# Kernel tuning notes

Hardware: AMD Instinct MI355X
Metric: run time of the kernel (lower is better)

## Reference

```python
import jax, jax.numpy as jnp
import numpy as np

N = 12500      # nodes
E = 200000     # edges (avg degree 16)
IN = 32        # inp_dim
OUT = 32       # out_dim
ATTN = 32      # attn_rel_emb_dim
R = 200        # num_rels
NB = 50        # num_bases


def setup_inputs() -> dict:
    key = jax.random.key(0)
    ks = jax.random.split(key, 10)
    node_feat = jax.random.normal(ks[0], (N, IN), jnp.float32)
    total_edge = jax.random.randint(ks[1], (2, E), 0, N)
    total_target_relation = jax.random.normal(ks[2], (E, ATTN), jnp.float32)
    total_relation_embed = jax.random.normal(ks[3], (E, ATTN), jnp.float32)
    total_relation = jax.random.randint(ks[4], (E,), 0, R)
    # learned parameters (xavier-ish scale)
    weight = jax.random.normal(ks[5], (NB, IN, OUT), jnp.float32) * 0.1
    w_comp = jax.random.normal(ks[6], (R, NB), jnp.float32) * 0.1
    self_loop_weight = jax.random.normal(ks[7], (IN, OUT), jnp.float32) * 0.1
    A_w = jax.random.normal(ks[8], (IN, 2 * IN + 2 * ATTN), jnp.float32) * 0.1
    A_b = jnp.zeros((IN,), jnp.float32)
    B_w = jax.random.normal(ks[9], (1, IN), jnp.float32) * 0.1
    B_b = jnp.zeros((1,), jnp.float32)
    return {
        'node_feat': node_feat,
        'total_target_relation': total_target_relation,
        'total_relation_embed': total_relation_embed,
        'weight': weight,
        'w_comp': w_comp,
        'self_loop_weight': self_loop_weight,
        'A_w': A_w,
        'A_b': A_b,
        'B_w': B_w,
        'B_b': B_b,
        'total_edge': total_edge,
        'total_relation': total_relation,
    }


def reference(node_feat, total_target_relation, total_relation_embed,
              weight, w_comp, self_loop_weight, A_w, A_b, B_w, B_b,
              total_edge, total_relation):
    # basis decomposition: per-relation weight [R, IN, OUT]
    rel_w = jnp.einsum('rb,bio->rio', w_comp, weight)
    src = node_feat[total_edge[0]]            # [E, IN]
    tgt = node_feat[total_edge[1]]            # [E, IN]
    # per-edge relation-specific transform (bmm in torch)
    msg = jnp.einsum('ei,eio->eo', src, rel_w[total_relation])  # [E, OUT]
    curr = tgt @ self_loop_weight             # [E, OUT]
    # attention MLP: sigmoid(B(relu(A(concat))))
    e = jnp.concatenate([src, tgt, total_relation_embed, total_target_relation], axis=1)
    h = jax.nn.relu(e @ A_w.T + A_b)
    a = jax.nn.sigmoid(h @ B_w.T + B_b)       # [E, 1]
    curr = curr + msg * a
    # gnn_spmm(e2n_sp, curr): scatter-add edge messages to target nodes
    out = jax.ops.segment_sum(curr, total_edge[1], num_segments=node_feat.shape[0])
    return out  # [N, OUT]
```

## Files before the change

kernel.cpp:

```cpp
#include <hip/hip_runtime.h>

#define N_NODES 12500
#define N_EDGES 200000
#define DIM 32
#define N_REL 200
#define N_BASES 50

#define OUT_ELEMS   (N_NODES * DIM)
#define ZERO_BLOCKS ((OUT_ELEMS + 1023) / 1024)

#define PE_MAX 203008
#define N_DUMMY_BLOCKS 8

#define NB_BLK 196
#define CHUNK 1024

#define HIST_BASE (N_REL + 1 + ZERO_BLOCKS)
#define PREP_BLOCKS (HIST_BASE + NB_BLK)
#define EDGE_BLOCKS (PE_MAX / 256)

#define AWBF_OFF  (N_REL * 1024 * 2)
#define SLWT_OFF  (AWBF_OFF + 32 * 128 * 2)
#define BCT_OFF   (SLWT_OFF + 32 * 32 * 2)
#define BBT_OFF   (BCT_OFF + N_REL * NB_BLK * 4)
#define OFFS_OFF  (BBT_OFF + N_REL * NB_BLK * 4)
#define TOTS_OFF  (OFFS_OFF + 816)
#define SLOT_OFF  (TOTS_OFF + 800)

typedef __attribute__((ext_vector_type(8))) short short8;
typedef __attribute__((ext_vector_type(4))) float f32x4;

__device__ __forceinline__ unsigned short f2bf(float x) {
    union { float f; unsigned u; } v; v.f = x;
    unsigned r = (v.u + 0x7FFFu + ((v.u >> 16) & 1u)) >> 16;
    return (unsigned short)r;
}

__device__ __forceinline__ short8 cvt8(float4 a, float4 b) {
    short8 r;
    r[0] = (short)f2bf(a.x); r[1] = (short)f2bf(a.y);
    r[2] = (short)f2bf(a.z); r[3] = (short)f2bf(a.w);
    r[4] = (short)f2bf(b.x); r[5] = (short)f2bf(b.y);
    r[6] = (short)f2bf(b.z); r[7] = (short)f2bf(b.w);
    return r;
}

#define MFMA(A, B, C) __builtin_amdgcn_mfma_f32_16x16x32_bf16(A, B, C, 0, 0, 0)

__global__ __launch_bounds__(256) void prep_kernel(
    const float* __restrict__ weight,
    const float* __restrict__ w_comp,
    const float* __restrict__ Aw,
    const float* __restrict__ slw,
    const int*  __restrict__ rel,
    unsigned short* __restrict__ relwT_bf,
    unsigned short* __restrict__ aw_bf,
    unsigned short* __restrict__ slwT_bf,
    int* __restrict__ blockCountsT,
    float* __restrict__ out)
{
    int b = blockIdx.x, tid = threadIdx.x;
    if (b < N_REL) {
        __shared__ float wc[N_BASES];
        if (tid < N_BASES) wc[tid] = w_comp[b * N_BASES + tid];
        __syncthreads();
        const float* wp = weight + tid * 4;
        float4 acc = make_float4(0.f, 0.f, 0.f, 0.f);
        #pragma unroll 10
        for (int bb = 0; bb < N_BASES; bb++) {
            float4 w = *(const float4*)(wp + bb * 1024);
            float c = wc[bb];
            acc.x = fmaf(c, w.x, acc.x); acc.y = fmaf(c, w.y, acc.y);
            acc.z = fmaf(c, w.z, acc.z); acc.w = fmaf(c, w.w, acc.w);
        }
        int i  = tid >> 3;
        int o0 = (tid * 4) & 31;
        unsigned short* dst = relwT_bf + b * 1024 + i;
        dst[(o0 + 0) * 32] = f2bf(acc.x);
        dst[(o0 + 1) * 32] = f2bf(acc.y);
        dst[(o0 + 2) * 32] = f2bf(acc.z);
        dst[(o0 + 3) * 32] = f2bf(acc.w);
    } else if (b == N_REL) {
        for (int x = tid; x < 32 * 128; x += 256) aw_bf[x] = f2bf(Aw[x]);
        for (int x = tid; x < 32 * 32; x += 256) {
            int i = x >> 5, j = x & 31;
            slwT_bf[j * 32 + i] = f2bf(slw[x]);
        }
    } else if (b < HIST_BASE) {
        int base = (b - (N_REL + 1)) * 1024 + tid * 4;
        if (base + 3 < OUT_ELEMS)
            *(float4*)(out + base) = make_float4(0.f, 0.f, 0.f, 0.f);
        else
            for (int k = 0; k < 4; k++)
                if (base + k < OUT_ELEMS) out[base + k] = 0.f;
    } else {
        __shared__ int h[N_REL];
        int blk = b - HIST_BASE;
        for (int x = tid; x < N_REL; x += 256) h[x] = 0;
        __syncthreads();
        int e0 = blk * CHUNK;
        int e1 = e0 + CHUNK; if (e1 > N_EDGES) e1 = N_EDGES;
        for (int e = e0 + tid; e < e1; e += 256) {
            int r = rel[e]; r = r < 0 ? 0 : (r >= N_REL ? N_REL - 1 : r);
            atomicAdd(&h[r], 1);
        }
        __syncthreads();
        for (int x = tid; x < N_REL; x += 256)
            blockCountsT[x * NB_BLK + blk] = h[x];
    }
}

__global__ __launch_bounds__(256) void scan_kernel(
    const int* __restrict__ blockCountsT,
    int* __restrict__ blockBaseT,
    int* __restrict__ offs, int* __restrict__ tots)
{
    __shared__ int s0[256];
    __shared__ int pval[256];
    int tid = threadIdx.x;
    int tot = 0;
    if (tid < N_REL) {
        const int4* cp = (const int4*)(blockCountsT + tid * NB_BLK);
        #pragma unroll 7
        for (int b = 0; b < NB_BLK / 4; b++) {
            int4 c = cp[b];
            tot += c.x + c.y + c.z + c.w;
        }
    }
    int p = (tid < N_REL) ? ((tot + 15) & ~15) : 0;
    pval[tid] = p;
    s0[tid] = p;
    __syncthreads();
    #pragma unroll
    for (int d = 1; d < 256; d <<= 1) {
        int v = s0[tid];
        if (tid >= d) v += s0[tid - d];
        __syncthreads();
        s0[tid] = v;
        __syncthreads();
    }
    int off = s0[tid] - pval[tid];
    if (tid < N_REL) { offs[tid] = off; tots[tid] = tot; }
    if (tid == 255) offs[N_REL] = s0[255];
    if (tid < N_REL) {
        const int4* cp = (const int4*)(blockCountsT + tid * NB_BLK);
        int4* bp = (int4*)(blockBaseT + tid * NB_BLK);
        int run = off;
        #pragma unroll 7
        for (int b = 0; b < NB_BLK / 4; b++) {
            int4 c = cp[b];
            int4 w;
            w.x = run;
            w.y = w.x + c.x;
            w.z = w.y + c.y;
            w.w = w.z + c.z;
            run = w.w + c.w;
            bp[b] = w;
        }
    }
}

__global__ __launch_bounds__(256) void gatescatter_kernel(
    const float* __restrict__ node_feat,
    const float* __restrict__ ttr,
    const float* __restrict__ tre,
    const float* __restrict__ Ab,
    const float* __restrict__ Bw,
    const float* __restrict__ Bb,
    const int*  __restrict__ edge0,
    const int*  __restrict__ edge1,
    const int*  __restrict__ rel,
    const unsigned short* __restrict__ aw_bf,
    const int* __restrict__ blockBaseT,
    const int* __restrict__ offs, const int* __restrict__ tots,
    int4* __restrict__ slot4)
{
    int b = blockIdx.x, tid = threadIdx.x;
    if (b >= NB_BLK) {
        int db = b - NB_BLK;
        const int4 dummy = make_int4(0, -1, 0, 0);
        for (int r = db; r < N_REL; r += N_DUMMY_BLOCKS) {
            int start = offs[r] + tots[r];
            int end   = offs[r] + ((tots[r] + 15) & ~15);
            for (int j = start + tid; j < end; j += 256)
                slot4[j] = dummy;
        }
        int padTotal = offs[N_REL];
        for (int j = padTotal + db * 256 + tid; j < PE_MAX; j += N_DUMMY_BLOCKS * 256)
            slot4[j] = dummy;
        return;
    }

    __shared__ int cur[N_REL];
    for (int x = tid; x < N_REL; x += 256)
        cur[x] = blockBaseT[x * NB_BLK + b];
    __syncthreads();

    int wave = tid >> 6;
    int lane = tid & 63;
    int m = lane & 15;
    int q = lane >> 4;

    short8 bA[4][2];
    #pragma unroll
    for (int hh = 0; hh < 2; hh++)
        #pragma unroll
        for (int c = 0; c < 4; c++)
            bA[c][hh] = *(const short8*)(aw_bf + (16 * hh + m) * 128 + 32 * c + 8 * q);
    float ab0 = Ab[m], ab1 = Ab[16 + m];
    float bw0 = Bw[m], bw1 = Bw[16 + m], Bb0 = Bb[0];

    int c0 = b * CHUNK;
    int cend = c0 + CHUNK; if (cend > N_EDGES) cend = N_EDGES;
    for (int it = 0; it < CHUNK / 256; it++) {
        int ebase = c0 + it * 256 + wave * 64;
        if (ebase >= cend) continue;

        int e_lane = ebase + lane;
        int s_ld = edge0[e_lane]; s_ld = s_ld < 0 ? 0 : (s_ld >= N_NODES ? N_NODES - 1 : s_ld);
        int t_ld = edge1[e_lane]; t_ld = t_ld < 0 ? 0 : (t_ld >= N_NODES ? N_NODES - 1 : t_ld);
        int r_ld = rel[e_lane];   r_ld = r_ld < 0 ? 0 : (r_ld >= N_REL   ? N_REL   - 1 : r_ld);

        short8 fsrc[4], ftgt[4], fre_[4], ftr_[4];
        #pragma unroll
        for (int g = 0; g < 4; g++) {
            int s_m = __shfl(s_ld, g * 16 + m, 64);
            int t_m = __shfl(t_ld, g * 16 + m, 64);
            int e_m = ebase + g * 16 + m;
            const float* sp = node_feat + s_m * DIM + q * 8;
            float4 sv0 = *(const float4*)sp, sv1 = *(const float4*)(sp + 4);
            const float* tp = node_feat + t_m * DIM + q * 8;
            float4 tv0 = *(const float4*)tp, tv1 = *(const float4*)(tp + 4);
            const float* rp = tre + e_m * DIM + q * 8;
            float4 rv0 = *(const float4*)rp, rv1 = *(const float4*)(rp + 4);
            const float* qp = ttr + e_m * DIM + q * 8;
            float4 qv0 = *(const float4*)qp, qv1 = *(const float4*)(qp + 4);
            fsrc[g] = cvt8(sv0, sv1);
            ftgt[g] = cvt8(tv0, tv1);
            fre_[g] = cvt8(rv0, rv1);
            ftr_[g] = cvt8(qv0, qv1);
        }

        #pragma unroll
        for (int g = 0; g < 4; g++) {
            f32x4 h0 = {ab0, ab0, ab0, ab0};
            f32x4 h1 = {ab1, ab1, ab1, ab1};
            h0 = MFMA(fsrc[g], bA[0][0], h0);  h1 = MFMA(fsrc[g], bA[0][1], h1);
            h0 = MFMA(ftgt[g], bA[1][0], h0);  h1 = MFMA(ftgt[g], bA[1][1], h1);
            h0 = MFMA(fre_[g], bA[2][0], h0);  h1 = MFMA(fre_[g], bA[2][1], h1);
            h0 = MFMA(ftr_[g], bA[3][0], h0);  h1 = MFMA(ftr_[g], bA[3][1], h1);

            float av[4];
            #pragma unroll
            for (int v = 0; v < 4; v++) {
                float p = fmaxf(h0[v], 0.f) * bw0 + fmaxf(h1[v], 0.f) * bw1;
                p += __shfl_xor(p, 1, 16);
                p += __shfl_xor(p, 2, 16);
                p += __shfl_xor(p, 4, 16);
                p += __shfl_xor(p, 8, 16);
                av[v] = 1.f / (1.f + __expf(-(p + Bb0)));
            }
            int j = g * 16 + 4 * q + m;
            int s_j = __shfl(s_ld, j, 64);
            int t_j = __shfl(t_ld, j, 64);
            int r_j = __shfl(r_ld, j, 64);
            float a_j = (m == 0) ? av[0] : (m == 1) ? av[1]
                      : (m == 2) ? av[2] : av[3];
            if (m < 4) {
                int pos = atomicAdd(&cur[r_j], 1);
                slot4[pos] = make_int4(s_j, t_j, __float_as_int(a_j), r_j);
            }
        }
    }
}

__global__ __launch_bounds__(256) void edge_kernel(
    const float* __restrict__ node_feat,
    const int4* __restrict__ slot4,
    const unsigned short* __restrict__ relwT_bf,
    const unsigned short* __restrict__ slwT_bf,
    float* __restrict__ out)
{
    int tid  = threadIdx.x;
    int wave = tid >> 6;
    int lane = tid & 63;
    int m = lane & 15;
    int q = lane >> 4;
    int wbase = blockIdx.x * 256 + wave * 64;

    int4 v = slot4[wbase + lane];
    int s_ld = v.x, t_ld = v.y, a_ld = v.z, r_ld = v.w;

    short8 bS[2];
    bS[0] = *(const short8*)(slwT_bf + m * 32 + 8 * q);
    bS[1] = *(const short8*)(slwT_bf + (16 + m) * 32 + 8 * q);

    short8 fsrc[4], ftgt[4], bM[4][2];
    #pragma unroll
    for (int g = 0; g < 4; g++) {
        int r_g = __shfl(r_ld, g * 16, 64);
        int s_m = __shfl(s_ld, g * 16 + m, 64);
        int t_m = __shfl(t_ld, g * 16 + m, 64);
        int t_mc = t_m < 0 ? 0 : t_m;
        const float* sp = node_feat + s_m * DIM + q * 8;
        float4 sv0 = *(const float4*)sp, sv1 = *(const float4*)(sp + 4);
        const float* tp = node_feat + t_mc * DIM + q * 8;
        float4 tv0 = *(const float4*)tp, tv1 = *(const float4*)(tp + 4);
        fsrc[g] = cvt8(sv0, sv1);
        ftgt[g] = cvt8(tv0, tv1);
        bM[g][0] = *(const short8*)(relwT_bf + r_g * 1024 + m * 32 + 8 * q);
        bM[g][1] = *(const short8*)(relwT_bf + r_g * 1024 + (16 + m) * 32 + 8 * q);
    }

    #pragma unroll
    for (int g = 0; g < 4; g++) {
        f32x4 m0 = {0.f, 0.f, 0.f, 0.f};
        f32x4 m1 = {0.f, 0.f, 0.f, 0.f};
        f32x4 c0 = {0.f, 0.f, 0.f, 0.f};
        f32x4 c1 = {0.f, 0.f, 0.f, 0.f};
        m0 = MFMA(fsrc[g], bM[g][0], m0);
        m1 = MFMA(fsrc[g], bM[g][1], m1);
        c0 = MFMA(ftgt[g], bS[0], c0);
        c1 = MFMA(ftgt[g], bS[1], c1);
        #pragma unroll
        for (int vv = 0; vv < 4; vv++) {
            int row = 4 * q + vv;
            int tv = __shfl(t_ld, g * 16 + row, 64);
            float a_row = __int_as_float(__shfl(a_ld, g * 16 + row, 64));
            if (tv >= 0) {
                atomicAdd(&out[tv * DIM + m],      c0[vv] + m0[vv] * a_row);
                atomicAdd(&out[tv * DIM + 16 + m], c1[vv] + m1[vv] * a_row);
            }
        }
    }
}

extern "C" void kernel_launch(void* const* d_in, const int* in_sizes, int n_in,
                              void* d_out, int out_size, void* d_ws, size_t ws_size,
                              hipStream_t stream) {
    const float* node_feat = (const float*)d_in[0];
    const float* ttr       = (const float*)d_in[1];
    const float* tre       = (const float*)d_in[2];
    const float* weight    = (const float*)d_in[3];
    const float* w_comp    = (const float*)d_in[4];
    const float* slw       = (const float*)d_in[5];
    const float* Aw        = (const float*)d_in[6];
    const float* Ab        = (const float*)d_in[7];
    const float* Bw        = (const float*)d_in[8];
    const float* Bb        = (const float*)d_in[9];
    const int*  total_edge = (const int*)d_in[10];
    const int*  rel        = (const int*)d_in[11];
    const int*  edge0 = total_edge;
    const int*  edge1 = total_edge + N_EDGES;

    char* ws = (char*)d_ws;
    unsigned short* relwT_bf = (unsigned short*)ws;
    unsigned short* aw_bf    = (unsigned short*)(ws + AWBF_OFF);
    unsigned short* slwT_bf  = (unsigned short*)(ws + SLWT_OFF);
    int*  blockCountsT = (int*)(ws + BCT_OFF);
    int*  blockBaseT   = (int*)(ws + BBT_OFF);
    int*  offs         = (int*)(ws + OFFS_OFF);
    int*  tots         = (int*)(ws + TOTS_OFF);
    int4* slot4        = (int4*)(ws + SLOT_OFF);
    float* out = (float*)d_out;

    prep_kernel<<<PREP_BLOCKS, 256, 0, stream>>>(
        weight, w_comp, Aw, slw, rel, relwT_bf, aw_bf, slwT_bf,
        blockCountsT, out);

    scan_kernel<<<1, 256, 0, stream>>>(blockCountsT, blockBaseT, offs, tots);

    gatescatter_kernel<<<NB_BLK + N_DUMMY_BLOCKS, 256, 0, stream>>>(
        node_feat, ttr, tre, Ab, Bw, Bb, edge0, edge1, rel,
        aw_bf, blockBaseT, offs, tots, slot4);

    edge_kernel<<<EDGE_BLOCKS, 256, 0, stream>>>(
        node_feat, slot4, relwT_bf, slwT_bf, out);
}
```

Measured before the change: 172.3 us.

## Fuse scan, gate/scatter and edge kernels into one persistent kernel

Merges the scan, the gate/scatter pass and the edge MFMA pass into a single persistent kernel of 256 blocks. Block 0 does the scan and publishes a flag. The other blocks compute attention gates into shared memory while the scan runs, then scatter edges into relation-sorted slots, pass a global atomic barrier, and finish the edge transform with a grid-stride loop. It also re-chunks the edges into 241 chunks of 832 to balance work. The aim is to remove two kernel launches and overlap the scan with the gate computation, at the cost of spin-wait barriers that need all blocks to be co-resident.

```diff
diff --git a/kernel.cpp b/kernel.cpp
--- a/kernel.cpp
+++ b/kernel.cpp
@@ -7,25 +7,31 @@
 #define N_BASES 50
 
 #define OUT_ELEMS   (N_NODES * DIM)
-#define ZERO_BLOCKS ((OUT_ELEMS + 1023) / 1024)
+#define ZERO_BLOCKS 391
 
 #define PE_MAX 203008
-#define N_DUMMY_BLOCKS 8
-
-#define NB_BLK 196
-#define CHUNK 1024
+
+#define CPG 13
+#define CHUNK (CPG * 64)
+#define NGROUPS 3125
+#define NB_CHUNK 241
+#define NB_PAD 244
+
+#define MEGA_BLK 256
+#define EDGE_UNITS (PE_MAX / 64)
+#define N_DUMMY_WRITERS (MEGA_BLK - NB_CHUNK)
 
 #define HIST_BASE (N_REL + 1 + ZERO_BLOCKS)
-#define PREP_BLOCKS (HIST_BASE + NB_BLK)
-#define EDGE_BLOCKS (PE_MAX / 256)
+#define PREP_BLOCKS (HIST_BASE + NB_CHUNK)
 
 #define AWBF_OFF  (N_REL * 1024 * 2)
 #define SLWT_OFF  (AWBF_OFF + 32 * 128 * 2)
 #define BCT_OFF   (SLWT_OFF + 32 * 32 * 2)
-#define BBT_OFF   (BCT_OFF + N_REL * NB_BLK * 4)
-#define OFFS_OFF  (BBT_OFF + N_REL * NB_BLK * 4)
+#define BBT_OFF   (BCT_OFF + N_REL * NB_PAD * 4)
+#define OFFS_OFF  (BBT_OFF + N_REL * NB_PAD * 4)
 #define TOTS_OFF  (OFFS_OFF + 816)
-#define SLOT_OFF  (TOTS_OFF + 800)
+#define FLAG_OFF  (TOTS_OFF + 800)
+#define SLOT_OFF  (FLAG_OFF + 16)
 
 typedef __attribute__((ext_vector_type(8))) short short8;
 typedef __attribute__((ext_vector_type(4))) float f32x4;
@@ -57,6 +63,7 @@
     unsigned short* __restrict__ aw_bf,
     unsigned short* __restrict__ slwT_bf,
     int* __restrict__ blockCountsT,
+    int* __restrict__ flags,
     float* __restrict__ out)
 {
     int b = blockIdx.x, tid = threadIdx.x;
@@ -86,6 +93,11 @@
             int i = x >> 5, j = x & 31;
             slwT_bf[j * 32 + i] = f2bf(slw[x]);
         }
+        if (tid < 4) flags[tid] = 0;
+        for (int x = tid; x < N_REL * (NB_PAD - NB_CHUNK); x += 256) {
+            int r = x / (NB_PAD - NB_CHUNK), p = x % (NB_PAD - NB_CHUNK);
+            blockCountsT[r * NB_PAD + NB_CHUNK + p] = 0;
+        }
     } else if (b < HIST_BASE) {
         int base = (b - (N_REL + 1)) * 1024 + tid * 4;
         if (base + 3 < OUT_ELEMS)
@@ -95,10 +107,10 @@
                 if (base + k < OUT_ELEMS) out[base + k] = 0.f;
     } else {
         __shared__ int h[N_REL];
-        int blk = b - HIST_BASE;
+        int c = b - HIST_BASE;
         for (int x = tid; x < N_REL; x += 256) h[x] = 0;
         __syncthreads();
-        int e0 = blk * CHUNK;
+        int e0 = c * CHUNK;
         int e1 = e0 + CHUNK; if (e1 > N_EDGES) e1 = N_EDGES;
         for (int e = e0 + tid; e < e1; e += 256) {
             int r = rel[e]; r = r < 0 ? 0 : (r >= N_REL ? N_REL - 1 : r);
@@ -106,61 +118,11 @@
         }
         __syncthreads();
         for (int x = tid; x < N_REL; x += 256)
-            blockCountsT[x * NB_BLK + blk] = h[x];
+            blockCountsT[x * NB_PAD + c] = h[x];
     }
 }
 
-__global__ __launch_bounds__(256) void scan_kernel(
-    const int* __restrict__ blockCountsT,
-    int* __restrict__ blockBaseT,
-    int* __restrict__ offs, int* __restrict__ tots)
-{
-    __shared__ int s0[256];
-    __shared__ int pval[256];
-    int tid = threadIdx.x;
-    int tot = 0;
-    if (tid < N_REL) {
-        const int4* cp = (const int4*)(blockCountsT + tid * NB_BLK);
-        #pragma unroll 7
-        for (int b = 0; b < NB_BLK / 4; b++) {
-            int4 c = cp[b];
-            tot += c.x + c.y + c.z + c.w;
-        }
-    }
-    int p = (tid < N_REL) ? ((tot + 15) & ~15) : 0;
-    pval[tid] = p;
-    s0[tid] = p;
-    __syncthreads();
-    #pragma unroll
-    for (int d = 1; d < 256; d <<= 1) {
-        int v = s0[tid];
-        if (tid >= d) v += s0[tid - d];
-        __syncthreads();
-        s0[tid] = v;
-        __syncthreads();
-    }
-    int off = s0[tid] - pval[tid];
-    if (tid < N_REL) { offs[tid] = off; tots[tid] = tot; }
-    if (tid == 255) offs[N_REL] = s0[255];
-    if (tid < N_REL) {
-        const int4* cp = (const int4*)(blockCountsT + tid * NB_BLK);
-        int4* bp = (int4*)(blockBaseT + tid * NB_BLK);
-        int run = off;
-        #pragma unroll 7
-        for (int b = 0; b < NB_BLK / 4; b++) {
-            int4 c = cp[b];
-            int4 w;
-            w.x = run;
-            w.y = w.x + c.x;
-            w.z = w.y + c.y;
-            w.w = w.z + c.z;
-            run = w.w + c.w;
-            bp[b] = w;
-        }
-    }
-}
-
-__global__ __launch_bounds__(256) void gatescatter_kernel(
+__global__ __launch_bounds__(256, 2) void mega_kernel(
     const float* __restrict__ node_feat,
     const float* __restrict__ ttr,
     const float* __restrict__ tre,
@@ -171,165 +133,231 @@
     const int*  __restrict__ edge1,
     const int*  __restrict__ rel,
     const unsigned short* __restrict__ aw_bf,
-    const int* __restrict__ blockBaseT,
-    const int* __restrict__ offs, const int* __restrict__ tots,
-    int4* __restrict__ slot4)
+    const unsigned short* __restrict__ relwT_bf,
+    const unsigned short* __restrict__ slwT_bf,
+    const int* __restrict__ blockCountsT,
+    int* __restrict__ blockBaseT,
+    int* __restrict__ offs, int* __restrict__ tots,
+    int* __restrict__ flags,
+    int4* __restrict__ slot4,
+    float* __restrict__ out)
 {
     int b = blockIdx.x, tid = threadIdx.x;
-    if (b >= NB_BLK) {
-        int db = b - NB_BLK;
+    int wave = tid >> 6;
+    int lane = tid & 63;
+    int m = lane & 15;
+    int q = lane >> 4;
+
+    __shared__ float a_stash[CHUNK];
+    __shared__ int   cur[N_REL];
+    __shared__ int   s0[256];
+    __shared__ int   pval[256];
+
+    int* scanflag = flags;
+    int* bar      = flags + 1;
+
+    if (b == 0) {
+        int tot = 0;
+        if (tid < N_REL) {
+            const int4* cp = (const int4*)(blockCountsT + tid * NB_PAD);
+            for (int c = 0; c < NB_PAD / 4; c++) {
+                int4 v = cp[c];
+                tot += v.x + v.y + v.z + v.w;
+            }
+        }
+        int p = (tid < N_REL) ? ((tot + 15) & ~15) : 0;
+        pval[tid] = p;
+        s0[tid] = p;
+        __syncthreads();
+        #pragma unroll
+        for (int d = 1; d < 256; d <<= 1) {
+            int v = s0[tid];
+            if (tid >= d) v += s0[tid - d];
+            __syncthreads();
+            s0[tid] = v;
+            __syncthreads();
+        }
+        int off = s0[tid] - pval[tid];
+        if (tid < N_REL) { offs[tid] = off; tots[tid] = tot; }
+        if (tid == 255) offs[N_REL] = s0[255];
+        if (tid < N_REL) {
+            const int4* cp = (const int4*)(blockCountsT + tid * NB_PAD);
+            int4* bp = (int4*)(blockBaseT + tid * NB_PAD);
+            int run = off;
+            for (int c = 0; c < NB_PAD / 4; c++) {
+                int4 v = cp[c];
+                int4 w;
+                w.x = run;
+                w.y = w.x + v.x;
+                w.z = w.y + v.y;
+                w.w = w.z + v.z;
+                run = w.w + v.w;
+                bp[c] = w;
+            }
+        }
+        __syncthreads();
+        if (tid == 0) {
+            __threadfence();
+            __hip_atomic_store(scanflag, 1, __ATOMIC_RELEASE, __HIP_MEMORY_SCOPE_AGENT);
+        }
+    }
+
+    int g_lo = b * CPG;
+    int g_cnt = 0;
+    if (b < NB_CHUNK) {
+        g_cnt = NGROUPS - g_lo; if (g_cnt > CPG) g_cnt = CPG;
+
+        short8 bA[4][2];
+        #pragma unroll
+        for (int hh = 0; hh < 2; hh++)
+            #pragma unroll
+            for (int c = 0; c < 4; c++)
+                bA[c][hh] = *(const short8*)(aw_bf + (16 * hh + m) * 128 + 32 * c + 8 * q);
+        float ab0 = Ab[m], ab1 = Ab[16 + m];
+        float bw0 = Bw[m], bw1 = Bw[16 + m], Bb0 = Bb[0];
+
+        for (int gi = wave; gi < g_cnt; gi += 4) {
+            int ebase = (g_lo + gi) * 64;
+            int e_lane = ebase + lane;
+            int s_ld = edge0[e_lane]; s_ld = s_ld < 0 ? 0 : (s_ld >= N_NODES ? N_NODES - 1 : s_ld);
+            int t_ld = edge1[e_lane]; t_ld = t_ld < 0 ? 0 : (t_ld >= N_NODES ? N_NODES - 1 : t_ld);
+
+            short8 fsrc[4], ftgt[4], fre_[4], ftr_[4];
+            #pragma unroll
+            for (int g = 0; g < 4; g++) {
+                int s_m = __shfl(s_ld, g * 16 + m, 64);
+                int t_m = __shfl(t_ld, g * 16 + m, 64);
+                int e_m = ebase + g * 16 + m;
+                const float* sp = node_feat + s_m * DIM + q * 8;
+                float4 sv0 = *(const float4*)sp, sv1 = *(const float4*)(sp + 4);
+                const float* tp = node_feat + t_m * DIM + q * 8;
+                float4 tv0 = *(const float4*)tp, tv1 = *(const float4*)(tp + 4);
+                const float* rp = tre + e_m * DIM + q * 8;
+                float4 rv0 = *(const float4*)rp, rv1 = *(const float4*)(rp + 4);
+                const float* qp = ttr + e_m * DIM + q * 8;
+                float4 qv0 = *(const float4*)qp, qv1 = *(const float4*)(qp + 4);
+                fsrc[g] = cvt8(sv0, sv1);
+                ftgt[g] = cvt8(tv0, tv1);
+                fre_[g] = cvt8(rv0, rv1);
+                ftr_[g] = cvt8(qv0, qv1);
+            }
+
+            #pragma unroll
+            for (int g = 0; g < 4; g++) {
+                f32x4 h0 = {ab0, ab0, ab0, ab0};
+                f32x4 h1 = {ab1, ab1, ab1, ab1};
+                h0 = MFMA(fsrc[g], bA[0][0], h0);  h1 = MFMA(fsrc[g], bA[0][1], h1);
+                h0 = MFMA(ftgt[g], bA[1][0], h0);  h1 = MFMA(ftgt[g], bA[1][1], h1);
+                h0 = MFMA(fre_[g], bA[2][0], h0);  h1 = MFMA(fre_[g], bA[2][1], h1);
+                h0 = MFMA(ftr_[g], bA[3][0], h0);  h1 = MFMA(ftr_[g], bA[3][1], h1);
+
+                float av[4];
+                #pragma unroll
+                for (int v = 0; v < 4; v++) {
+                    float p = fmaxf(h0[v], 0.f) * bw0 + fmaxf(h1[v], 0.f) * bw1;
+                    p += __shfl_xor(p, 1, 16);
+                    p += __shfl_xor(p, 2, 16);
+                    p += __shfl_xor(p, 4, 16);
+                    p += __shfl_xor(p, 8, 16);
+                    av[v] = 1.f / (1.f + __expf(-(p + Bb0)));
+                }
+                float a_j = (m == 0) ? av[0] : (m == 1) ? av[1]
+                          : (m == 2) ? av[2] : av[3];
+                if (m < 4) a_stash[gi * 64 + g * 16 + 4 * q + m] = a_j;
+            }
+        }
+    }
+
+    __syncthreads();
+    if (tid == 0)
+        while (__hip_atomic_load(scanflag, __ATOMIC_ACQUIRE, __HIP_MEMORY_SCOPE_AGENT) == 0)
+            __builtin_amdgcn_s_sleep(2);
+    __syncthreads();
+    __threadfence();
+
+    if (b < NB_CHUNK) {
+        for (int x = tid; x < N_REL; x += 256)
+            cur[x] = blockBaseT[x * NB_PAD + b];
+        __syncthreads();
+        int c0 = g_lo * 64;
+        int clen = g_cnt * 64;
+        for (int ei = tid; ei < clen; ei += 256) {
+            int e = c0 + ei;
+            int r = rel[e];   r = r < 0 ? 0 : (r >= N_REL   ? N_REL   - 1 : r);
+            int s = edge0[e]; s = s < 0 ? 0 : (s >= N_NODES ? N_NODES - 1 : s);
+            int t = edge1[e]; t = t < 0 ? 0 : (t >= N_NODES ? N_NODES - 1 : t);
+            int pos = atomicAdd(&cur[r], 1);
+            slot4[pos] = make_int4(s, t, __float_as_int(a_stash[ei]), r);
+        }
+    } else {
+        int db = b - NB_CHUNK;
         const int4 dummy = make_int4(0, -1, 0, 0);
-        for (int r = db; r < N_REL; r += N_DUMMY_BLOCKS) {
+        for (int r = db; r < N_REL; r += N_DUMMY_WRITERS) {
             int start = offs[r] + tots[r];
             int end   = offs[r] + ((tots[r] + 15) & ~15);
             for (int j = start + tid; j < end; j += 256)
                 slot4[j] = dummy;
         }
         int padTotal = offs[N_REL];
-        for (int j = padTotal + db * 256 + tid; j < PE_MAX; j += N_DUMMY_BLOCKS * 256)
+        for (int j = padTotal + db * 256 + tid; j < PE_MAX; j += N_DUMMY_WRITERS * 256)
             slot4[j] = dummy;
-        return;
-    }
-
-    __shared__ int cur[N_REL];
-    for (int x = tid; x < N_REL; x += 256)
-        cur[x] = blockBaseT[x * NB_BLK + b];
+    }
+
     __syncthreads();
-
-    int wave = tid >> 6;
-    int lane = tid & 63;
-    int m = lane & 15;
-    int q = lane >> 4;
-
-    short8 bA[4][2];
-    #pragma unroll
-    for (int hh = 0; hh < 2; hh++)
-        #pragma unroll
-        for (int c = 0; c < 4; c++)
-            bA[c][hh] = *(const short8*)(aw_bf + (16 * hh + m) * 128 + 32 * c + 8 * q);
-    float ab0 = Ab[m], ab1 = Ab[16 + m];
-    float bw0 = Bw[m], bw1 = Bw[16 + m], Bb0 = Bb[0];
-
-    int c0 = b * CHUNK;
-    int cend = c0 + CHUNK; if (cend > N_EDGES) cend = N_EDGES;
-    for (int it = 0; it < CHUNK / 256; it++) {
-        int ebase = c0 + it * 256 + wave * 64;
-        if (ebase >= cend) continue;
-
-        int e_lane = ebase + lane;
-        int s_ld = edge0[e_lane]; s_ld = s_ld < 0 ? 0 : (s_ld >= N_NODES ? N_NODES - 1 : s_ld);
-        int t_ld = edge1[e_lane]; t_ld = t_ld < 0 ? 0 : (t_ld >= N_NODES ? N_NODES - 1 : t_ld);
-        int r_ld = rel[e_lane];   r_ld = r_ld < 0 ? 0 : (r_ld >= N_REL   ? N_REL   - 1 : r_ld);
-
-        short8 fsrc[4], ftgt[4], fre_[4], ftr_[4];
-        #pragma unroll
-        for (int g = 0; g < 4; g++) {
-            int s_m = __shfl(s_ld, g * 16 + m, 64);
-            int t_m = __shfl(t_ld, g * 16 + m, 64);
-            int e_m = ebase + g * 16 + m;
-            const float* sp = node_feat + s_m * DIM + q * 8;
-            float4 sv0 = *(const float4*)sp, sv1 = *(const float4*)(sp + 4);
-            const float* tp = node_feat + t_m * DIM + q * 8;
-            float4 tv0 = *(const float4*)tp, tv1 = *(const float4*)(tp + 4);
-            const float* rp = tre + e_m * DIM + q * 8;
-            float4 rv0 = *(const float4*)rp, rv1 = *(const float4*)(rp + 4);
-            const float* qp = ttr + e_m * DIM + q * 8;
-            float4 qv0 = *(const float4*)qp, qv1 = *(const float4*)(qp + 4);
-            fsrc[g] = cvt8(sv0, sv1);
-            ftgt[g] = cvt8(tv0, tv1);
-            fre_[g] = cvt8(rv0, rv1);
-            ftr_[g] = cvt8(qv0, qv1);
-        }
-
-        #pragma unroll
-        for (int g = 0; g < 4; g++) {
-            f32x4 h0 = {ab0, ab0, ab0, ab0};
-            f32x4 h1 = {ab1, ab1, ab1, ab1};
-            h0 = MFMA(fsrc[g], bA[0][0], h0);  h1 = MFMA(fsrc[g], bA[0][1], h1);
-            h0 = MFMA(ftgt[g], bA[1][0], h0);  h1 = MFMA(ftgt[g], bA[1][1], h1);
-            h0 = MFMA(fre_[g], bA[2][0], h0);  h1 = MFMA(fre_[g], bA[2][1], h1);
-            h0 = MFMA(ftr_[g], bA[3][0], h0);  h1 = MFMA(ftr_[g], bA[3][1], h1);
-
-            float av[4];
-            #pragma unroll
-            for (int v = 0; v < 4; v++) {
-                float p = fmaxf(h0[v], 0.f) * bw0 + fmaxf(h1[v], 0.f) * bw1;
-                p += __shfl_xor(p, 1, 16);
-                p += __shfl_xor(p, 2, 16);
-                p += __shfl_xor(p, 4, 16);
-                p += __shfl_xor(p, 8, 16);
-                av[v] = 1.f / (1.f + __expf(-(p + Bb0)));
-            }
-            int j = g * 16 + 4 * q + m;
-            int s_j = __shfl(s_ld, j, 64);
-            int t_j = __shfl(t_ld, j, 64);
-            int r_j = __shfl(r_ld, j, 64);
-            float a_j = (m == 0) ? av[0] : (m == 1) ? av[1]
-                      : (m == 2) ? av[2] : av[3];
-            if (m < 4) {
-                int pos = atomicAdd(&cur[r_j], 1);
-                slot4[pos] = make_int4(s_j, t_j, __float_as_int(a_j), r_j);
-            }
-        }
-    }
-}
-
-__global__ __launch_bounds__(256) void edge_kernel(
-    const float* __restrict__ node_feat,
-    const int4* __restrict__ slot4,
-    const unsigned short* __restrict__ relwT_bf,
-    const unsigned short* __restrict__ slwT_bf,
-    float* __restrict__ out)
-{
-    int tid  = threadIdx.x;
-    int wave = tid >> 6;
-    int lane = tid & 63;
-    int m = lane & 15;
-    int q = lane >> 4;
-    int wbase = blockIdx.x * 256 + wave * 64;
-
-    int4 v = slot4[wbase + lane];
-    int s_ld = v.x, t_ld = v.y, a_ld = v.z, r_ld = v.w;
+    if (tid == 0) {
+        __threadfence();
+        __hip_atomic_fetch_add(bar, 1, __ATOMIC_ACQ_REL, __HIP_MEMORY_SCOPE_AGENT);
+        while (__hip_atomic_load(bar, __ATOMIC_ACQUIRE, __HIP_MEMORY_SCOPE_AGENT) < MEGA_BLK)
+            __builtin_amdgcn_s_sleep(2);
+    }
+    __syncthreads();
+    __threadfence();
 
     short8 bS[2];
     bS[0] = *(const short8*)(slwT_bf + m * 32 + 8 * q);
     bS[1] = *(const short8*)(slwT_bf + (16 + m) * 32 + 8 * q);
 
-    short8 fsrc[4], ftgt[4], bM[4][2];
-    #pragma unroll
-    for (int g = 0; g < 4; g++) {
-        int r_g = __shfl(r_ld, g * 16, 64);
-        int s_m = __shfl(s_ld, g * 16 + m, 64);
-        int t_m = __shfl(t_ld, g * 16 + m, 64);
-        int t_mc = t_m < 0 ? 0 : t_m;
-        const float* sp = node_feat + s_m * DIM + q * 8;
-        float4 sv0 = *(const float4*)sp, sv1 = *(const float4*)(sp + 4);
-        const float* tp = node_feat + t_mc * DIM + q * 8;
-        float4 tv0 = *(const float4*)tp, tv1 = *(const float4*)(tp + 4);
-        fsrc[g] = cvt8(sv0, sv1);
-        ftgt[g] = cvt8(tv0, tv1);
-        bM[g][0] = *(const short8*)(relwT_bf + r_g * 1024 + m * 32 + 8 * q);
-        bM[g][1] = *(const short8*)(relwT_bf + r_g * 1024 + (16 + m) * 32 + 8 * q);
-    }
-
-    #pragma unroll
-    for (int g = 0; g < 4; g++) {
-        f32x4 m0 = {0.f, 0.f, 0.f, 0.f};
-        f32x4 m1 = {0.f, 0.f, 0.f, 0.f};
-        f32x4 c0 = {0.f, 0.f, 0.f, 0.f};
-        f32x4 c1 = {0.f, 0.f, 0.f, 0.f};
-        m0 = MFMA(fsrc[g], bM[g][0], m0);
-        m1 = MFMA(fsrc[g], bM[g][1], m1);
-        c0 = MFMA(ftgt[g], bS[0], c0);
-        c1 = MFMA(ftgt[g], bS[1], c1);
+    for (int u = b * 4 + wave; u < EDGE_UNITS; u += MEGA_BLK * 4) {
+        int wbase = u * 64;
+        int4 v = slot4[wbase + lane];
+        int s_ld = v.x, t_ld = v.y, a_ld = v.z, r_ld = v.w;
+
+        short8 fsrc[4], ftgt[4], bM[4][2];
         #pragma unroll
-        for (int vv = 0; vv < 4; vv++) {
-            int row = 4 * q + vv;
-            int tv = __shfl(t_ld, g * 16 + row, 64);
-            float a_row = __int_as_float(__shfl(a_ld, g * 16 + row, 64));
-            if (tv >= 0) {
-                atomicAdd(&out[tv * DIM + m],      c0[vv] + m0[vv] * a_row);
-                atomicAdd(&out[tv * DIM + 16 + m], c1[vv] + m1[vv] * a_row);
+        for (int g = 0; g < 4; g++) {
+            int r_g = __shfl(r_ld, g * 16, 64);
+            int s_m = __shfl(s_ld, g * 16 + m, 64);
+            int t_m = __shfl(t_ld, g * 16 + m, 64);
+            int t_mc = t_m < 0 ? 0 : t_m;
+            const float* sp = node_feat + s_m * DIM + q * 8;
+            float4 sv0 = *(const float4*)sp, sv1 = *(const float4*)(sp + 4);
+            const float* tp = node_feat + t_mc * DIM + q * 8;
+            float4 tv0 = *(const float4*)tp, tv1 = *(const float4*)(tp + 4);
+            fsrc[g] = cvt8(sv0, sv1);
+            ftgt[g] = cvt8(tv0, tv1);
+            bM[g][0] = *(const short8*)(relwT_bf + r_g * 1024 + m * 32 + 8 * q);
+            bM[g][1] = *(const short8*)(relwT_bf + r_g * 1024 + (16 + m) * 32 + 8 * q);
+        }
+
+        #pragma unroll
+        for (int g = 0; g < 4; g++) {
+            f32x4 m0 = {0.f, 0.f, 0.f, 0.f};
+            f32x4 m1 = {0.f, 0.f, 0.f, 0.f};
+            f32x4 c0 = {0.f, 0.f, 0.f, 0.f};
+            f32x4 c1 = {0.f, 0.f, 0.f, 0.f};
+            m0 = MFMA(fsrc[g], bM[g][0], m0);
+            m1 = MFMA(fsrc[g], bM[g][1], m1);
+            c0 = MFMA(ftgt[g], bS[0], c0);
+            c1 = MFMA(ftgt[g], bS[1], c1);
+            #pragma unroll
+            for (int vv = 0; vv < 4; vv++) {
+                int row = 4 * q + vv;
+                int tv = __shfl(t_ld, g * 16 + row, 64);
+                float a_row = __int_as_float(__shfl(a_ld, g * 16 + row, 64));
+                if (tv >= 0) {
+                    atomicAdd(&out[tv * DIM + m],      c0[vv] + m0[vv] * a_row);
+                    atomicAdd(&out[tv * DIM + 16 + m], c1[vv] + m1[vv] * a_row);
+                }
             }
         }
     }
@@ -361,19 +389,16 @@
     int*  blockBaseT   = (int*)(ws + BBT_OFF);
     int*  offs         = (int*)(ws + OFFS_OFF);
     int*  tots         = (int*)(ws + TOTS_OFF);
+    int*  flags        = (int*)(ws + FLAG_OFF);
     int4* slot4        = (int4*)(ws + SLOT_OFF);
     float* out = (float*)d_out;
 
     prep_kernel<<<PREP_BLOCKS, 256, 0, stream>>>(
         weight, w_comp, Aw, slw, rel, relwT_bf, aw_bf, slwT_bf,
-        blockCountsT, out);
-
-    scan_kernel<<<1, 256, 0, stream>>>(blockCountsT, blockBaseT, offs, tots);
-
-    gatescatter_kernel<<<NB_BLK + N_DUMMY_BLOCKS, 256, 0, stream>>>(
+        blockCountsT, flags, out);
+
+    mega_kernel<<<MEGA_BLK, 256, 0, stream>>>(
         node_feat, ttr, tre, Ab, Bw, Bb, edge0, edge1, rel,
-        aw_bf, blockBaseT, offs, tots, slot4);
-
-    edge_kernel<<<EDGE_BLOCKS, 256, 0, stream>>>(
-        node_feat, slot4, relwT_bf, slwT_bf, out);
+        aw_bf, relwT_bf, slwT_bf, blockCountsT, blockBaseT,
+        offs, tots, flags, slot4, out);
 }
```

Result: slower. 347.2 us (+101.6%).
